# Kernel optimization log

Hardware: AMD Instinct MI355X
Metric: run time of the kernel (lower is better)

## Reference

```python
import jax, jax.numpy as jnp
import numpy as np

NUM_CLASSES = 2
THRESHOLD = 0.35   # overlap_thresh
NEG_POS = 7        # negative:positive mining ratio
VAR0, VAR1 = 0.1, 0.2  # self.variance


def point_form(boxes):
    # (cx,cy,w,h) -> (xmin,ymin,xmax,ymax); boxes [P,4]
    return jnp.concatenate([boxes[:, :2] - boxes[:, 2:] / 2,
                            boxes[:, :2] + boxes[:, 2:] / 2], axis=1)


def jaccard(box_a, box_b):
    # box_a [B,O,4] xyxy, box_b [P,4] xyxy -> IoU [B,O,P]
    max_xy = jnp.minimum(box_a[:, :, None, 2:], box_b[None, None, :, 2:])
    min_xy = jnp.maximum(box_a[:, :, None, :2], box_b[None, None, :, :2])
    wh = jnp.clip(max_xy - min_xy, 0.0)
    inter = wh[..., 0] * wh[..., 1]
    area_a = ((box_a[..., 2] - box_a[..., 0]) * (box_a[..., 3] - box_a[..., 1]))[:, :, None]
    area_b = ((box_b[:, 2] - box_b[:, 0]) * (box_b[:, 3] - box_b[:, 1]))[None, None, :]
    return inter / (area_a + area_b - inter)


def encode(matched, priors):
    # matched [B,P,4] xyxy, priors [1,P,4] cxcywh -> offsets [B,P,4]
    g_cxcy = (matched[..., :2] + matched[..., 2:]) / 2 - priors[..., :2]
    g_cxcy = g_cxcy / (VAR0 * priors[..., 2:])
    g_wh = (matched[..., 2:] - matched[..., :2]) / priors[..., 2:]
    g_wh = jnp.log(g_wh) / VAR1
    return jnp.concatenate([g_cxcy, g_wh], axis=-1)


def match(truths, labels, priors):
    # truths [B,O,4] xyxy, labels [B,O] float, priors [P,4] cxcywh
    overlaps = jaccard(truths, point_form(priors))      # [B,O,P]
    best_prior_idx = jnp.argmax(overlaps, axis=2)       # [B,O] best prior per gt
    best_truth_overlap = jnp.max(overlaps, axis=1)      # [B,P]
    best_truth_idx = jnp.argmax(overlaps, axis=1)       # [B,P] best gt per prior
    O = truths.shape[1]

    def fix(bto, bti, bpi):
        # ensure every gt keeps its best prior (index_fill_ / loop in torch)
        bto = bto.at[bpi].set(2.0)
        bti = bti.at[bpi].set(jnp.arange(O))
        return bto, bti

    best_truth_overlap, best_truth_idx = jax.vmap(fix)(
        best_truth_overlap, best_truth_idx, best_prior_idx)
    matched = jnp.take_along_axis(truths, best_truth_idx[..., None], axis=1)  # [B,P,4]
    conf = jnp.take_along_axis(labels, best_truth_idx, axis=1).astype(jnp.int32) + 1
    conf = jnp.where(best_truth_overlap < THRESHOLD, 0, conf)  # background
    loc = encode(matched, priors[None])
    return loc, conf


def setup_inputs() -> dict:
    key = jax.random.key(0)
    k1, k2, k3, k4, k5, k6 = jax.random.split(key, 6)
    B, P, O, C = 32, 32768, 32, NUM_CLASSES
    loc_data = jax.random.normal(k1, (B, P, 4), jnp.float32)
    conf_data = jax.random.normal(k2, (B, P, C), jnp.float32)
    # priors: (cx,cy,w,h) in [0,1], wh in [0.02,0.3]
    p_cxcy = jax.random.uniform(k3, (P, 2), jnp.float32)
    p_wh = 0.02 + 0.28 * jax.random.uniform(k4, (P, 2), jnp.float32)
    priors = jnp.concatenate([p_cxcy, p_wh], axis=1)
    # targets: valid xyxy boxes + label column (label 0 -> class 1 after +1)
    t_cxcy = 0.1 + 0.8 * jax.random.uniform(k5, (B, O, 2), jnp.float32)
    t_wh = 0.05 + 0.2 * jax.random.uniform(k6, (B, O, 2), jnp.float32)
    boxes = jnp.concatenate([t_cxcy - t_wh / 2, t_cxcy + t_wh / 2], axis=2)
    labels = jnp.zeros((B, O, 1), jnp.float32)
    targets = jnp.concatenate([boxes, labels], axis=2)
    return {"loc_data": loc_data, "conf_data": conf_data,
            "priors": priors, "targets": targets}


def reference(loc_data, conf_data, priors, targets):
    B, P, C = conf_data.shape
    truths = targets[..., :4]
    labels = targets[..., 4]
    loc_t, conf_t = match(truths, labels, priors)   # [B,P,4], [B,P] int
    pos = conf_t > 0                                # [B,P]

    # localization: smooth-L1 summed over positives
    diff = loc_data - loc_t
    ad = jnp.abs(diff)
    sl1 = jnp.where(ad < 1.0, 0.5 * diff * diff, ad - 0.5)
    loss_l = jnp.sum(sl1 * pos[..., None].astype(loc_data.dtype))

    # per-prior CE loss for hard-negative mining
    lse = jax.nn.logsumexp(conf_data, axis=2)                            # [B,P]
    picked = jnp.take_along_axis(conf_data, conf_t[..., None], axis=2)[..., 0]
    ce = lse - picked                                                    # [B,P]
    mine = jnp.where(pos, 0.0, ce)
    # double-argsort rank trick (descending)
    loss_idx = jnp.argsort(-mine, axis=1)
    idx_rank = jnp.argsort(loss_idx, axis=1)
    num_pos = jnp.sum(pos, axis=1, keepdims=True)                        # [B,1]
    num_neg = jnp.minimum(NEG_POS * num_pos, P - 1)
    neg = idx_rank < num_neg

    sel = pos | neg
    loss_c = jnp.sum(jnp.where(sel, ce, 0.0))

    N = jnp.maximum(jnp.sum(num_pos).astype(jnp.float32), 1.0)
    return loss_l / N, loss_c / N
```

## Files before the change

### kernel.cpp

```cpp
#include <hip/hip_runtime.h>
#include <stdint.h>

#define NB 32
#define NP 32768
#define NO 32
#define THRESH 0.35f
#define NT1 64
#define HCOL 33

typedef unsigned long long u64;
typedef unsigned int u32;

__device__ __forceinline__ float iou_corners(float px1, float py1, float px2, float py2, float ab,
                                             float tx1, float ty1, float tx2, float ty2, float aa)
{
#pragma clang fp contract(off)
    float iw = fminf(tx2, px2) - fmaxf(tx1, px1);
    float ih = fminf(ty2, py2) - fmaxf(ty1, py1);
    iw = fmaxf(iw, 0.f); ih = fmaxf(ih, 0.f);
    float inter = iw * ih;
    return __fdividef(inter, aa + ab - inter);
}

__device__ __forceinline__ float smooth_l1_sum(float4 ld, float4 pr, float4 tt)
{
#pragma clang fp contract(off)
    float g0 = __fdividef((tt.x + tt.z) * 0.5f - pr.x, 0.1f * pr.z);
    float g1 = __fdividef((tt.y + tt.w) * 0.5f - pr.y, 0.1f * pr.w);
    float g2 = __logf(__fdividef(tt.z - tt.x, pr.z)) * 5.0f;
    float g3 = __logf(__fdividef(tt.w - tt.y, pr.w)) * 5.0f;
    float d0 = ld.x - g0, d1 = ld.y - g1, d2 = ld.z - g2, d3 = ld.w - g3;
    float a0 = fabsf(d0), a1 = fabsf(d1), a2 = fabsf(d2), a3 = fabsf(d3);
    return (a0 < 1.f ? 0.5f * d0 * d0 : a0 - 0.5f)
         + (a1 < 1.f ? 0.5f * d1 * d1 : a1 - 0.5f)
         + (a2 < 1.f ? 0.5f * d2 * d2 : a2 - 0.5f)
         + (a3 < 1.f ? 0.5f * d3 * d3 : a3 - 0.5f);
}

__device__ __forceinline__ float lse2(float c0, float c1)
{
#pragma clang fp contract(off)
    float mm = fmaxf(c0, c1), mn = fminf(c0, c1);
    return mm + __logf(1.f + __expf(mn - mm));
}

__global__ __launch_bounds__(256) void kern1(
        const float* __restrict__ loc, const float* __restrict__ conf,
        const float* __restrict__ priors, const float* __restrict__ targets,
        float* __restrict__ mine, u64* __restrict__ bpk_part,
        float* __restrict__ part_sl1, float* __restrict__ part_cep, int* __restrict__ part_np,
        float* __restrict__ sl_tot, float* __restrict__ c_tot,
        int* __restrict__ np_tot, int* __restrict__ done_cnt)
{
#pragma clang fp contract(off)
    __shared__ __align__(16) float4 tbc[NO];
    __shared__ float ta[NO], tlab[NO];
    __shared__ u64 keys[NO];
    __shared__ float rs0[4], rs1[4];
    __shared__ int rc[4];
    const int b = blockIdx.y, x = blockIdx.x, tid = threadIdx.x;
    if (b == 0 && x == 0 && tid == 0) {
        *sl_tot = 0.f; *c_tot = 0.f; *np_tot = 0; *done_cnt = 0;
    }
    if (tid < NO * 5) {
        int o = tid / 5, c = tid % 5;
        float v = targets[b * NO * 5 + tid];
        if (c < 4) ((float*)&tbc[o])[c] = v; else tlab[o] = v;
    }
    if (tid < NO) keys[tid] = 0ull;
    __syncthreads();
    if (tid < NO) {
        float4 t = tbc[tid];
        ta[tid] = (t.z - t.x) * (t.w - t.y);
    }
    __syncthreads();

    const int p0 = x * 512 + tid * 2;
    float4 pr[2];
    float px1[2], py1[2], px2[2], py2[2], ab[2];
#pragma unroll
    for (int j = 0; j < 2; ++j) {
        pr[j] = ((const float4*)priors)[p0 + j];
        px1[j] = pr[j].x - pr[j].z * 0.5f;
        py1[j] = pr[j].y - pr[j].w * 0.5f;
        px2[j] = pr[j].x + pr[j].z * 0.5f;
        py2[j] = pr[j].y + pr[j].w * 0.5f;
        ab[j]  = pr[j].z * pr[j].w;
    }
    u64 bk[2] = {0ull, 0ull};
    const int lane_o = tid & 31;
    for (int it = 0; it < NO; ++it) {
        const int o = (it + lane_o) & 31;
        float4 tt = tbc[o];
        float aa = ta[o];
        float iou2[2];
#pragma unroll
        for (int j = 0; j < 2; ++j) {
            float iou = iou_corners(px1[j], py1[j], px2[j], py2[j], ab[j],
                                    tt.x, tt.y, tt.z, tt.w, aa);
            iou2[j] = iou;
            u64 ko = ((u64)__float_as_uint(iou) << 6) | (u64)(63 - o);
            bk[j] = bk[j] > ko ? bk[j] : ko;
        }
        float vm = fmaxf(iou2[0], iou2[1]);
        u64 cur = keys[o];
        if (__float_as_uint(vm) > (u32)(cur >> 32)) {
            float bi = iou2[1]; int bp = p0 + 1;
            if (iou2[0] >= bi) { bi = iou2[0]; bp = p0; }
            atomicMax(&keys[o], ((u64)__float_as_uint(bi) << 32) | (u64)(~(u32)bp));
        }
    }

    const size_t gbase = (size_t)b * NP + p0;
    float4 cf = ((const float4*)conf)[gbase >> 1];
    float c0[2] = {cf.x, cf.z};
    float c1[2] = {cf.y, cf.w};
    float2 mout;
    float s_sl1 = 0.f, s_cep = 0.f;
    int np = 0;
#pragma unroll
    for (int j = 0; j < 2; ++j) {
        u32 vb = (u32)(bk[j] >> 6);
        float bv = __uint_as_float(vb);
        int o = 63 - (int)(bk[j] & 63);
        int cfv = (bv < THRESH) ? 0 : ((int)tlab[o] + 1);
        bool pos = cfv > 0;
        float4 ld = ((const float4*)loc)[gbase + j];
        float sl1 = smooth_l1_sum(ld, pr[j], tbc[o]);
        float ce = lse2(c0[j], c1[j]) - ((cfv == 0) ? c0[j] : c1[j]);
        if (pos) { s_sl1 += sl1; s_cep += ce; np++; }
        ((float*)&mout)[j] = pos ? 0.f : ce;
    }
    ((float2*)mine)[gbase >> 1] = mout;

#pragma unroll
    for (int m = 32; m; m >>= 1) {
        s_sl1 += __shfl_xor(s_sl1, m, 64);
        s_cep += __shfl_xor(s_cep, m, 64);
        np    += __shfl_xor(np, m, 64);
    }
    int lane = tid & 63, w = tid >> 6;
    if (lane == 0) { rs0[w] = s_sl1; rs1[w] = s_cep; rc[w] = np; }
    __syncthreads();
    if (tid == 0) {
        float t0 = 0.f, t1 = 0.f; int t2 = 0;
        for (int i = 0; i < 4; ++i) { t0 += rs0[i]; t1 += rs1[i]; t2 += rc[i]; }
        part_sl1[b * NT1 + x] = t0;
        part_cep[b * NT1 + x] = t1;
        part_np [b * NT1 + x] = t2;
    }
    if (tid < NO) bpk_part[(b * NT1 + x) * 32 + tid] = keys[tid];
}

__global__ __launch_bounds__(1024) void kern3(
        const float* __restrict__ loc, const float* __restrict__ conf,
        const float* __restrict__ priors, const float* __restrict__ targets,
        const u64* __restrict__ bpk_part, const float* __restrict__ mine,
        const float* __restrict__ part_sl1, const float* __restrict__ part_cep,
        const int* __restrict__ part_np,
        float* __restrict__ sl_tot, float* __restrict__ c_tot,
        int* __restrict__ np_tot, int* __restrict__ done_cnt,
        float* __restrict__ out)
{
#pragma clang fp contract(off)
    const int b = blockIdx.x, tid = threadIdx.x;
    const int wave = tid >> 6, lane = tid & 63;
    const int cl = lane & 31;
    __shared__ __align__(16) float4 tbc[NO];
    __shared__ float tlab[NO], tas[NO];
    __shared__ u32 pp[NO];
    __shared__ u32 flags[1024];
    __shared__ int hA[256 * HCOL], hB[256 * HCOL];
    __shared__ int wtot[4];
    __shared__ float rs[16];
    __shared__ int rc2[16];
    __shared__ float sh_sl1, sh_cep;
    __shared__ int sh_np, sh_k, sh_kk;
    __shared__ u32 sh_prefix;

    if (tid < NO * 5) {
        int o = tid / 5, c = tid % 5;
        float v = targets[b * NO * 5 + tid];
        if (c < 4) ((float*)&tbc[o])[c] = v; else tlab[o] = v;
    }
    flags[tid] = 0u;
    for (int i = tid; i < 256 * HCOL; i += 1024) { hA[i] = 0; hB[i] = 0; }

    const float* mb = mine + (size_t)b * NP;
    float v[32];
#pragma unroll
    for (int q = 0; q < 8; ++q) {
        float4 t4 = ((const float4*)mb)[q * 1024 + tid];
        v[4 * q] = t4.x; v[4 * q + 1] = t4.y; v[4 * q + 2] = t4.z; v[4 * q + 3] = t4.w;
    }
    __syncthreads();

#pragma unroll 8
    for (int j = 0; j < 32; ++j)
        atomicAdd(&hA[(__float_as_uint(v[j]) >> 24) * HCOL + cl], 1);
    if (tid < NO) {
        float4 t = tbc[tid];
        tas[tid] = (t.z - t.x) * (t.w - t.y);
        u64 key = 0ull;
        for (int xx = 0; xx < NT1; ++xx) {
            u64 t2 = bpk_part[(b * NT1 + xx) * 32 + tid];
            key = t2 > key ? t2 : key;
        }
        pp[tid] = (key >> 32) ? ~(u32)key : 0u;
    }
    __syncthreads();

    if (tid < NO) {
        const int o = tid;
        const u32 p = pp[o];
        float dsl1 = 0.f, dcep = 0.f; int dnp = 0;
        bool last = true;
        for (int o2 = o + 1; o2 < NO; ++o2)
            if (pp[o2] == p) { last = false; break; }
        if (last) {
            float4 prr = ((const float4*)priors)[p];
            float px1 = prr.x - prr.z * 0.5f, py1 = prr.y - prr.w * 0.5f;
            float px2 = prr.x + prr.z * 0.5f, py2 = prr.y + prr.w * 0.5f;
            float ab = prr.z * prr.w;
            float bv = -1.f; int bo_ = 0;
            for (int o2 = 0; o2 < NO; ++o2) {
                float4 t2 = tbc[o2];
                float i2 = iou_corners(px1, py1, px2, py2, ab, t2.x, t2.y, t2.z, t2.w, tas[o2]);
                if (i2 > bv) { bv = i2; bo_ = o2; }
            }
            int cf_pre = (bv < THRESH) ? 0 : ((int)tlab[bo_] + 1);
            size_t gp = (size_t)b * NP + p;
            float4 ld = ((const float4*)loc)[gp];
            float2 c = ((const float2*)conf)[gp];
            float lse = lse2(c.x, c.y);
            int cf_new = (int)tlab[o] + 1;
            dsl1 = smooth_l1_sum(ld, prr, tbc[o]);
            dcep = lse - ((cf_new == 0) ? c.x : c.y);
            dnp = 1;
            if (cf_pre > 0) {
                dsl1 -= smooth_l1_sum(ld, prr, tbc[bo_]);
                dcep -= lse - ((cf_pre == 0) ? c.x : c.y);
                dnp = 0;
            }
            float oldv = mb[p];
            atomicSub(&hA[(__float_as_uint(oldv) >> 24) * HCOL + cl], 1);
            atomicAdd(&hA[cl], 1);
            atomicOr(&flags[p >> 5], 1u << (p & 31));
        }
        float a = part_sl1[b * NT1 + o] + part_sl1[b * NT1 + 32 + o] + dsl1;
        float d = part_cep[b * NT1 + o] + part_cep[b * NT1 + 32 + o] + dcep;
        int   n = part_np [b * NT1 + o] + part_np [b * NT1 + 32 + o] + dnp;
#pragma unroll
        for (int m = 16; m; m >>= 1) {
            a += __shfl_xor(a, m, 32);
            d += __shfl_xor(d, m, 32);
            n += __shfl_xor(n, m, 32);
        }
        if (o == 0) {
            sh_sl1 = a; sh_cep = d; sh_np = n;
            sh_k = min(7 * n, NP - 1); sh_kk = sh_k; sh_prefix = 0u;
        }
    }
    __syncthreads();

    const int k = sh_k;
    float topk = 0.f;
    if (k > 0) {
#pragma unroll
        for (int q = 0; q < 8; ++q) {
            u32 word = flags[q * 128 + (tid >> 3)];
#pragma unroll
            for (int c = 0; c < 4; ++c)
                if ((word >> (((tid & 7) << 2) + c)) & 1u) v[4 * q + c] = 0.f;
        }
        for (int pass = 0; pass < 4; ++pass) {
            int* cur = (pass & 1) ? hB : hA;
            if (pass > 0) {
                const int shift = 24 - 8 * pass;
                const u32 pfx = sh_prefix;
#pragma unroll 8
                for (int j = 0; j < 32; ++j) {
                    u32 kb = __float_as_uint(v[j]);
                    if ((u32)(((u64)kb) >> (shift + 8)) == pfx)
                        atomicAdd(&cur[((kb >> shift) & 255) * HCOL + cl], 1);
                }
                if (pass < 3) {
                    int* other = (pass & 1) ? hA : hB;
                    for (int i = tid; i < 256 * HCOL; i += 1024) other[i] = 0;
                }
                __syncthreads();
            }
            int tot = 0, suf = 0;
            if (tid < 256) {
                const int hb = tid * HCOL;
#pragma unroll
                for (int i = 0; i < HCOL; ++i) tot += cur[hb + i];
                suf = tot;
#pragma unroll
                for (int off = 1; off < 64; off <<= 1) {
                    int u = __shfl_down(suf, off, 64);
                    if (lane + off < 64) suf += u;
                }
                if (lane == 0) wtot[wave] = suf;
            }
            __syncthreads();
            if (tid < 256) {
                int excl = suf - tot;
                for (int w2 = wave + 1; w2 < 4; ++w2) excl += wtot[w2];
                int kk = sh_kk;
                if (excl < kk && kk <= excl + tot) {
                    sh_prefix = (sh_prefix << 8) | (u32)tid;
                    sh_kk = kk - excl;
                }
            }
            __syncthreads();
        }
        const u32 T = sh_prefix;
        const float tval = __uint_as_float(T);
        float ssum = 0.f; int c2 = 0;
#pragma unroll
        for (int j = 0; j < 32; ++j) {
            if (__float_as_uint(v[j]) > T) { ssum += v[j]; c2++; }
        }
#pragma unroll
        for (int m = 32; m; m >>= 1) {
            ssum += __shfl_xor(ssum, m, 64);
            c2   += __shfl_xor(c2, m, 64);
        }
        if (lane == 0) { rs[wave] = ssum; rc2[wave] = c2; }
        __syncthreads();
        if (tid == 0) {
            float st = 0.f; int ct = 0;
            for (int i = 0; i < 16; ++i) { st += rs[i]; ct += rc2[i]; }
            topk = st + (float)(k - ct) * tval;
        }
    }
    if (tid == 0) {
        atomicAdd(sl_tot, sh_sl1);
        atomicAdd(c_tot, sh_cep + topk);
        atomicAdd(np_tot, sh_np);
        __threadfence();
        int d = atomicAdd(done_cnt, 1);
        if (d == NB - 1) {
            float sl = atomicAdd(sl_tot, 0.f);
            float cc = atomicAdd(c_tot, 0.f);
            int   np = atomicAdd(np_tot, 0);
            float N = fmaxf((float)np, 1.f);
            out[0] = sl / N;
            out[1] = cc / N;
        }
    }
}

extern "C" void kernel_launch(void* const* d_in, const int* in_sizes, int n_in,
                              void* d_out, int out_size, void* d_ws, size_t ws_size,
                              hipStream_t stream) {
    const float* loc     = (const float*)d_in[0];
    const float* conf    = (const float*)d_in[1];
    const float* priors  = (const float*)d_in[2];
    const float* targets = (const float*)d_in[3];
    float* out = (float*)d_out;

    char* ws = (char*)d_ws;
    float* mine     = (float*)ws;
    u64*   bpk_part = (u64*)(ws + 4194304);
    float* part_sl1 = (float*)(ws + 4718592);
    float* part_cep = (float*)(ws + 4726784);
    int*   part_np  = (int*)(ws + 4734976);
    float* sl_tot   = (float*)(ws + 4743168);
    float* c_tot    = (float*)(ws + 4743172);
    int*   np_tot   = (int*)(ws + 4743176);
    int*   done_cnt = (int*)(ws + 4743180);

    dim3 g1(NT1, NB);
    kern1<<<g1, 256, 0, stream>>>(loc, conf, priors, targets, mine, bpk_part,
                                  part_sl1, part_cep, part_np,
                                  sl_tot, c_tot, np_tot, done_cnt);
    kern3<<<NB, 1024, 0, stream>>>(loc, conf, priors, targets, bpk_part, mine,
                                   part_sl1, part_cep, part_np,
                                   sl_tot, c_tot, np_tot, done_cnt, out);
}
```

Before: 127.2 us.

## Overlap per-gt fixup in one wave with histogram clearing in others

Restructures the start of kern3 so that one wave (wave 15) loads targets, reduces the bpk partials with a 64-lane split plus shuffle, and computes the per-gt fixup deltas. Meanwhile the other 15 waves clear the histograms. The forced-match flags are then applied to the mine values before building the first histogram, replacing the old atomic subtract/add correction, and one block-wide barrier is removed. The intent is to take the serial 32-thread section off the critical path. The cost is that all of that work now sits in a single wave.

```diff
diff --git a/kernel.cpp b/kernel.cpp
--- a/kernel.cpp
+++ b/kernel.cpp
@@ -168,9 +168,11 @@
     const int cl = lane & 31;
     __shared__ __align__(16) float4 tbc[NO];
     __shared__ float tlab[NO], tas[NO];
-    __shared__ u32 pp[NO];
+    __shared__ u32 pp_s[NO];
     __shared__ u32 flags[1024];
     __shared__ int hA[256 * HCOL], hB[256 * HCOL];
+    __shared__ float dslA[NO], dceA[NO];
+    __shared__ int dnpA[NO];
     __shared__ int wtot[4];
     __shared__ float rs[16];
     __shared__ int rc2[16];
@@ -178,14 +180,6 @@
     __shared__ int sh_np, sh_k, sh_kk;
     __shared__ u32 sh_prefix;
 
-    if (tid < NO * 5) {
-        int o = tid / 5, c = tid % 5;
-        float v = targets[b * NO * 5 + tid];
-        if (c < 4) ((float*)&tbc[o])[c] = v; else tlab[o] = v;
-    }
-    flags[tid] = 0u;
-    for (int i = tid; i < 256 * HCOL; i += 1024) { hA[i] = 0; hB[i] = 0; }
-
     const float* mb = mine + (size_t)b * NP;
     float v[32];
 #pragma unroll
@@ -193,70 +187,103 @@
         float4 t4 = ((const float4*)mb)[q * 1024 + tid];
         v[4 * q] = t4.x; v[4 * q + 1] = t4.y; v[4 * q + 2] = t4.z; v[4 * q + 3] = t4.w;
     }
+
+    if (wave < 15) {
+        for (int i = tid; i < 1024; i += 960) { }
+        for (int i = tid; i < 256 * HCOL; i += 960) { hA[i] = 0; hB[i] = 0; }
+    } else {
+        for (int i = lane; i < 1024; i += 64) flags[i] = 0u;
+        float tv0 = targets[b * NO * 5 + lane];
+        float tv1 = targets[b * NO * 5 + 64 + lane];
+        float tv2 = (lane < 32) ? targets[b * NO * 5 + 128 + lane] : 0.f;
+        const int ro = lane & 31, rh = lane >> 5;
+        const u64* bp = bpk_part + ((size_t)(b * NT1 + rh * 32)) * 32 + ro;
+        u64 key = 0ull;
+#pragma unroll
+        for (int j = 0; j < 32; ++j) {
+            u64 t2 = bp[(size_t)j * 32];
+            key = t2 > key ? t2 : key;
+        }
+        {
+            int e = lane;       int o = e / 5, c = e % 5;
+            if (c < 4) ((float*)&tbc[o])[c] = tv0; else tlab[o] = tv0;
+            e = lane + 64;      o = e / 5;  c = e % 5;
+            if (c < 4) ((float*)&tbc[o])[c] = tv1; else tlab[o] = tv1;
+            if (lane < 32) {
+                e = lane + 128; o = e / 5;  c = e % 5;
+                if (c < 4) ((float*)&tbc[o])[c] = tv2; else tlab[o] = tv2;
+            }
+        }
+        if (lane < NO) {
+            float4 t = tbc[lane];
+            tas[lane] = (t.z - t.x) * (t.w - t.y);
+        }
+        {
+            u64 t2 = __shfl_xor(key, 32, 64);
+            key = t2 > key ? t2 : key;
+        }
+        u32 ppv = (key >> 32) ? ~(u32)key : 0u;
+        if (lane < NO) pp_s[lane] = ppv;
+        if (lane < NO) {
+            const int o = lane;
+            const u32 p = ppv;
+            float dsl1 = 0.f, dcep = 0.f; int dnp = 0;
+            bool last = true;
+            for (int o2 = o + 1; o2 < NO; ++o2)
+                if (pp_s[o2] == p) { last = false; break; }
+            if (last) {
+                float4 prr = ((const float4*)priors)[p];
+                float px1 = prr.x - prr.z * 0.5f, py1 = prr.y - prr.w * 0.5f;
+                float px2 = prr.x + prr.z * 0.5f, py2 = prr.y + prr.w * 0.5f;
+                float ab = prr.z * prr.w;
+                float bv = -1.f; int bo_ = 0;
+                for (int o2 = 0; o2 < NO; ++o2) {
+                    float4 t2 = tbc[o2];
+                    float i2 = iou_corners(px1, py1, px2, py2, ab, t2.x, t2.y, t2.z, t2.w, tas[o2]);
+                    if (i2 > bv) { bv = i2; bo_ = o2; }
+                }
+                int cf_pre = (bv < THRESH) ? 0 : ((int)tlab[bo_] + 1);
+                size_t gp = (size_t)b * NP + p;
+                float4 ld = ((const float4*)loc)[gp];
+                float2 c = ((const float2*)conf)[gp];
+                float lse = lse2(c.x, c.y);
+                int cf_new = (int)tlab[o] + 1;
+                dsl1 = smooth_l1_sum(ld, prr, tbc[o]);
+                dcep = lse - ((cf_new == 0) ? c.x : c.y);
+                dnp = 1;
+                if (cf_pre > 0) {
+                    dsl1 -= smooth_l1_sum(ld, prr, tbc[bo_]);
+                    dcep -= lse - ((cf_pre == 0) ? c.x : c.y);
+                    dnp = 0;
+                }
+                atomicOr(&flags[p >> 5], 1u << (p & 31));
+            }
+            dslA[o] = dsl1; dceA[o] = dcep; dnpA[o] = dnp;
+        }
+    }
     __syncthreads();
 
+#pragma unroll
+    for (int q = 0; q < 8; ++q) {
+        u32 word = flags[q * 128 + (tid >> 3)];
+#pragma unroll
+        for (int c = 0; c < 4; ++c)
+            if ((word >> (((tid & 7) << 2) + c)) & 1u) v[4 * q + c] = 0.f;
+    }
 #pragma unroll 8
     for (int j = 0; j < 32; ++j)
         atomicAdd(&hA[(__float_as_uint(v[j]) >> 24) * HCOL + cl], 1);
     if (tid < NO) {
-        float4 t = tbc[tid];
-        tas[tid] = (t.z - t.x) * (t.w - t.y);
-        u64 key = 0ull;
-        for (int xx = 0; xx < NT1; ++xx) {
-            u64 t2 = bpk_part[(b * NT1 + xx) * 32 + tid];
-            key = t2 > key ? t2 : key;
-        }
-        pp[tid] = (key >> 32) ? ~(u32)key : 0u;
-    }
-    __syncthreads();
-
-    if (tid < NO) {
-        const int o = tid;
-        const u32 p = pp[o];
-        float dsl1 = 0.f, dcep = 0.f; int dnp = 0;
-        bool last = true;
-        for (int o2 = o + 1; o2 < NO; ++o2)
-            if (pp[o2] == p) { last = false; break; }
-        if (last) {
-            float4 prr = ((const float4*)priors)[p];
-            float px1 = prr.x - prr.z * 0.5f, py1 = prr.y - prr.w * 0.5f;
-            float px2 = prr.x + prr.z * 0.5f, py2 = prr.y + prr.w * 0.5f;
-            float ab = prr.z * prr.w;
-            float bv = -1.f; int bo_ = 0;
-            for (int o2 = 0; o2 < NO; ++o2) {
-                float4 t2 = tbc[o2];
-                float i2 = iou_corners(px1, py1, px2, py2, ab, t2.x, t2.y, t2.z, t2.w, tas[o2]);
-                if (i2 > bv) { bv = i2; bo_ = o2; }
-            }
-            int cf_pre = (bv < THRESH) ? 0 : ((int)tlab[bo_] + 1);
-            size_t gp = (size_t)b * NP + p;
-            float4 ld = ((const float4*)loc)[gp];
-            float2 c = ((const float2*)conf)[gp];
-            float lse = lse2(c.x, c.y);
-            int cf_new = (int)tlab[o] + 1;
-            dsl1 = smooth_l1_sum(ld, prr, tbc[o]);
-            dcep = lse - ((cf_new == 0) ? c.x : c.y);
-            dnp = 1;
-            if (cf_pre > 0) {
-                dsl1 -= smooth_l1_sum(ld, prr, tbc[bo_]);
-                dcep -= lse - ((cf_pre == 0) ? c.x : c.y);
-                dnp = 0;
-            }
-            float oldv = mb[p];
-            atomicSub(&hA[(__float_as_uint(oldv) >> 24) * HCOL + cl], 1);
-            atomicAdd(&hA[cl], 1);
-            atomicOr(&flags[p >> 5], 1u << (p & 31));
-        }
-        float a = part_sl1[b * NT1 + o] + part_sl1[b * NT1 + 32 + o] + dsl1;
-        float d = part_cep[b * NT1 + o] + part_cep[b * NT1 + 32 + o] + dcep;
-        int   n = part_np [b * NT1 + o] + part_np [b * NT1 + 32 + o] + dnp;
+        float a = part_sl1[b * NT1 + tid] + part_sl1[b * NT1 + 32 + tid] + dslA[tid];
+        float d = part_cep[b * NT1 + tid] + part_cep[b * NT1 + 32 + tid] + dceA[tid];
+        int   n = part_np [b * NT1 + tid] + part_np [b * NT1 + 32 + tid] + dnpA[tid];
 #pragma unroll
         for (int m = 16; m; m >>= 1) {
             a += __shfl_xor(a, m, 32);
             d += __shfl_xor(d, m, 32);
             n += __shfl_xor(n, m, 32);
         }
-        if (o == 0) {
+        if (tid == 0) {
             sh_sl1 = a; sh_cep = d; sh_np = n;
             sh_k = min(7 * n, NP - 1); sh_kk = sh_k; sh_prefix = 0u;
         }
@@ -266,13 +293,6 @@
     const int k = sh_k;
     float topk = 0.f;
     if (k > 0) {
-#pragma unroll
-        for (int q = 0; q < 8; ++q) {
-            u32 word = flags[q * 128 + (tid >> 3)];
-#pragma unroll
-            for (int c = 0; c < 4; ++c)
-                if ((word >> (((tid & 7) << 2) + c)) & 1u) v[4 * q + c] = 0.f;
-        }
         for (int pass = 0; pass < 4; ++pass) {
             int* cur = (pass & 1) ? hB : hA;
             if (pass > 0) {
```

Result: no change. 126.3 us (-0.7%).

## Fuse match and hard-negative top-k kernels via last-block-per-batch completion counter

Applied to the files above, without the earlier changes.

Merges the per-prior matching kernel and the per-batch top-k selection kernel into one launch. Each 1024-thread block covers four 512-prior tiles, and the last block to finish a batch (found with an atomic counter) runs the radix-select top-k by re-reading the mining buffer from global memory instead of holding it in registers. Loc loads are also skipped for non-positive priors, and counters are cleared with a memset. The aim is to remove the second launch and the inter-kernel gap, at the cost of large shared memory per block (lower occupancy in the matching phase), repeated global reads during radix passes, and a serialized tail per batch.

```diff
diff --git a/kernel.cpp b/kernel.cpp
--- a/kernel.cpp
+++ b/kernel.cpp
@@ -6,10 +6,14 @@
 #define NO 32
 #define THRESH 0.35f
 #define NT1 64
+#define GR 16
 #define HCOL 33
 
 typedef unsigned long long u64;
 typedef unsigned int u32;
+
+#define AGLD(p)    __hip_atomic_load((p), __ATOMIC_RELAXED, __HIP_MEMORY_SCOPE_AGENT)
+#define AGST(p, v) __hip_atomic_store((p), (v), __ATOMIC_RELAXED, __HIP_MEMORY_SCOPE_AGENT)
 
 __device__ __forceinline__ float iou_corners(float px1, float py1, float px2, float py2, float ab,
                                              float tx1, float ty1, float tx2, float ty2, float aa)
@@ -44,38 +48,46 @@
     return mm + __logf(1.f + __expf(mn - mm));
 }
 
-__global__ __launch_bounds__(256) void kern1(
+__global__ __launch_bounds__(1024) void kfused(
         const float* __restrict__ loc, const float* __restrict__ conf,
         const float* __restrict__ priors, const float* __restrict__ targets,
         float* __restrict__ mine, u64* __restrict__ bpk_part,
         float* __restrict__ part_sl1, float* __restrict__ part_cep, int* __restrict__ part_np,
         float* __restrict__ sl_tot, float* __restrict__ c_tot,
-        int* __restrict__ np_tot, int* __restrict__ done_cnt)
+        int* __restrict__ np_tot, int* __restrict__ done_cnt,
+        int* __restrict__ batch_cnt, float* __restrict__ out)
 {
 #pragma clang fp contract(off)
     __shared__ __align__(16) float4 tbc[NO];
-    __shared__ float ta[NO], tlab[NO];
-    __shared__ u64 keys[NO];
-    __shared__ float rs0[4], rs1[4];
-    __shared__ int rc[4];
-    const int b = blockIdx.y, x = blockIdx.x, tid = threadIdx.x;
-    if (b == 0 && x == 0 && tid == 0) {
-        *sl_tot = 0.f; *c_tot = 0.f; *np_tot = 0; *done_cnt = 0;
-    }
+    __shared__ float tlab[NO], tas[NO];
+    __shared__ u64 keys[4][NO];
+    __shared__ float rs0[16], rs1[16];
+    __shared__ int rc[16];
+    __shared__ __align__(16) int hA[256 * HCOL];
+    __shared__ __align__(16) int hB[256 * HCOL];
+    __shared__ u32 flags[1024];
+    __shared__ u32 pp_s[NO];
+    __shared__ int wtot[4];
+    __shared__ float rs[16];
+    __shared__ int rc2[16];
+    __shared__ float sh_sl1, sh_cep;
+    __shared__ int sh_np, sh_k, sh_kk, sh_done;
+    __shared__ u32 sh_prefix;
+
+    const int b = blockIdx.y, g = blockIdx.x, tid = threadIdx.x;
+    const int unit = tid >> 8, ut = tid & 255;
+    const int x = g * 4 + unit;
+    const int lane = tid & 63, wv = tid >> 6;
+
     if (tid < NO * 5) {
         int o = tid / 5, c = tid % 5;
         float v = targets[b * NO * 5 + tid];
         if (c < 4) ((float*)&tbc[o])[c] = v; else tlab[o] = v;
     }
-    if (tid < NO) keys[tid] = 0ull;
-    __syncthreads();
-    if (tid < NO) {
-        float4 t = tbc[tid];
-        ta[tid] = (t.z - t.x) * (t.w - t.y);
-    }
-    __syncthreads();
-
-    const int p0 = x * 512 + tid * 2;
+    if (tid < NO * 4) ((u64*)keys)[tid] = 0ull;
+    __syncthreads();
+
+    const int p0 = x * 512 + ut * 2;
     float4 pr[2];
     float px1[2], py1[2], px2[2], py2[2], ab[2];
 #pragma unroll
@@ -88,11 +100,11 @@
         ab[j]  = pr[j].z * pr[j].w;
     }
     u64 bk[2] = {0ull, 0ull};
-    const int lane_o = tid & 31;
+    const int lane_o = ut & 31;
     for (int it = 0; it < NO; ++it) {
         const int o = (it + lane_o) & 31;
         float4 tt = tbc[o];
-        float aa = ta[o];
+        float aa = (tt.z - tt.x) * (tt.w - tt.y);
         float iou2[2];
 #pragma unroll
         for (int j = 0; j < 2; ++j) {
@@ -103,11 +115,11 @@
             bk[j] = bk[j] > ko ? bk[j] : ko;
         }
         float vm = fmaxf(iou2[0], iou2[1]);
-        u64 cur = keys[o];
+        u64 cur = keys[unit][o];
         if (__float_as_uint(vm) > (u32)(cur >> 32)) {
             float bi = iou2[1]; int bp = p0 + 1;
             if (iou2[0] >= bi) { bi = iou2[0]; bp = p0; }
-            atomicMax(&keys[o], ((u64)__float_as_uint(bi) << 32) | (u64)(~(u32)bp));
+            atomicMax(&keys[unit][o], ((u64)__float_as_uint(bi) << 32) | (u64)(~(u32)bp));
         }
     }
 
@@ -115,7 +127,7 @@
     float4 cf = ((const float4*)conf)[gbase >> 1];
     float c0[2] = {cf.x, cf.z};
     float c1[2] = {cf.y, cf.w};
-    float2 mout;
+    float mo0 = 0.f, mo1 = 0.f;
     float s_sl1 = 0.f, s_cep = 0.f;
     int np = 0;
 #pragma unroll
@@ -125,13 +137,17 @@
         int o = 63 - (int)(bk[j] & 63);
         int cfv = (bv < THRESH) ? 0 : ((int)tlab[o] + 1);
         bool pos = cfv > 0;
-        float4 ld = ((const float4*)loc)[gbase + j];
-        float sl1 = smooth_l1_sum(ld, pr[j], tbc[o]);
         float ce = lse2(c0[j], c1[j]) - ((cfv == 0) ? c0[j] : c1[j]);
-        if (pos) { s_sl1 += sl1; s_cep += ce; np++; }
-        ((float*)&mout)[j] = pos ? 0.f : ce;
-    }
-    ((float2*)mine)[gbase >> 1] = mout;
+        if (pos) {
+            float4 ld = ((const float4*)loc)[gbase + j];
+            s_sl1 += smooth_l1_sum(ld, pr[j], tbc[o]);
+            s_cep += ce;
+            np++;
+        }
+        if (j == 0) mo0 = pos ? 0.f : ce; else mo1 = pos ? 0.f : ce;
+    }
+    AGST((u64*)mine + (gbase >> 1),
+         ((u64)__float_as_uint(mo0)) | (((u64)__float_as_uint(mo1)) << 32));
 
 #pragma unroll
     for (int m = 32; m; m >>= 1) {
@@ -139,93 +155,58 @@
         s_cep += __shfl_xor(s_cep, m, 64);
         np    += __shfl_xor(np, m, 64);
     }
-    int lane = tid & 63, w = tid >> 6;
-    if (lane == 0) { rs0[w] = s_sl1; rs1[w] = s_cep; rc[w] = np; }
+    if (lane == 0) { rs0[wv] = s_sl1; rs1[wv] = s_cep; rc[wv] = np; }
+    __syncthreads();
+    if (ut == 0) {
+        float t0 = 0.f, t1 = 0.f; int t2 = 0;
+        for (int i = 0; i < 4; ++i) { t0 += rs0[unit * 4 + i]; t1 += rs1[unit * 4 + i]; t2 += rc[unit * 4 + i]; }
+        AGST(&part_sl1[b * NT1 + x], t0);
+        AGST(&part_cep[b * NT1 + x], t1);
+        AGST(&part_np [b * NT1 + x], t2);
+    }
+    if (ut < NO) AGST(&bpk_part[(b * NT1 + x) * 32 + ut], keys[unit][ut]);
     __syncthreads();
     if (tid == 0) {
-        float t0 = 0.f, t1 = 0.f; int t2 = 0;
-        for (int i = 0; i < 4; ++i) { t0 += rs0[i]; t1 += rs1[i]; t2 += rc[i]; }
-        part_sl1[b * NT1 + x] = t0;
-        part_cep[b * NT1 + x] = t1;
-        part_np [b * NT1 + x] = t2;
-    }
-    if (tid < NO) bpk_part[(b * NT1 + x) * 32 + tid] = keys[tid];
-}
-
-__global__ __launch_bounds__(1024) void kern3(
-        const float* __restrict__ loc, const float* __restrict__ conf,
-        const float* __restrict__ priors, const float* __restrict__ targets,
-        const u64* __restrict__ bpk_part, const float* __restrict__ mine,
-        const float* __restrict__ part_sl1, const float* __restrict__ part_cep,
-        const int* __restrict__ part_np,
-        float* __restrict__ sl_tot, float* __restrict__ c_tot,
-        int* __restrict__ np_tot, int* __restrict__ done_cnt,
-        float* __restrict__ out)
-{
-#pragma clang fp contract(off)
-    const int b = blockIdx.x, tid = threadIdx.x;
-    const int wave = tid >> 6, lane = tid & 63;
-    const int cl = lane & 31;
-    __shared__ __align__(16) float4 tbc[NO];
-    __shared__ float tlab[NO], tas[NO];
-    __shared__ u32 pp[NO];
-    __shared__ u32 flags[1024];
-    __shared__ int hA[256 * HCOL], hB[256 * HCOL];
-    __shared__ int wtot[4];
-    __shared__ float rs[16];
-    __shared__ int rc2[16];
-    __shared__ float sh_sl1, sh_cep;
-    __shared__ int sh_np, sh_k, sh_kk;
-    __shared__ u32 sh_prefix;
-
-    if (tid < NO * 5) {
-        int o = tid / 5, c = tid % 5;
-        float v = targets[b * NO * 5 + tid];
-        if (c < 4) ((float*)&tbc[o])[c] = v; else tlab[o] = v;
-    }
+        __threadfence();
+        sh_done = atomicAdd(&batch_cnt[b], 1);
+    }
+    __syncthreads();
+    if (sh_done != GR - 1) return;
+    __threadfence();
+
     flags[tid] = 0u;
-    for (int i = tid; i < 256 * HCOL; i += 1024) { hA[i] = 0; hB[i] = 0; }
-
-    const float* mb = mine + (size_t)b * NP;
-    float v[32];
-#pragma unroll
-    for (int q = 0; q < 8; ++q) {
-        float4 t4 = ((const float4*)mb)[q * 1024 + tid];
-        v[4 * q] = t4.x; v[4 * q + 1] = t4.y; v[4 * q + 2] = t4.z; v[4 * q + 3] = t4.w;
-    }
-    __syncthreads();
-
-#pragma unroll 8
-    for (int j = 0; j < 32; ++j)
-        atomicAdd(&hA[(__float_as_uint(v[j]) >> 24) * HCOL + cl], 1);
+    for (int i = tid; i < 256 * HCOL; i += 1024) hA[i] = 0;
+    {
+        u64* scr = (u64*)hB;
+        int o = tid & 31, ch = tid >> 5;
+        u64 a = AGLD(&bpk_part[(b * NT1 + 2 * ch) * 32 + o]);
+        u64 c2 = AGLD(&bpk_part[(b * NT1 + 2 * ch + 1) * 32 + o]);
+        scr[o * 32 + ch] = a > c2 ? a : c2;
+    }
+    __syncthreads();
     if (tid < NO) {
+        u64* scr = (u64*)hB;
+        u64 key = 0ull;
+        for (int ch = 0; ch < 32; ++ch) { u64 t2 = scr[tid * 32 + ch]; key = t2 > key ? t2 : key; }
         float4 t = tbc[tid];
         tas[tid] = (t.z - t.x) * (t.w - t.y);
-        u64 key = 0ull;
-        for (int xx = 0; xx < NT1; ++xx) {
-            u64 t2 = bpk_part[(b * NT1 + xx) * 32 + tid];
-            key = t2 > key ? t2 : key;
-        }
-        pp[tid] = (key >> 32) ? ~(u32)key : 0u;
-    }
-    __syncthreads();
-
-    if (tid < NO) {
+        u32 ppv = (key >> 32) ? ~(u32)key : 0u;
+        pp_s[tid] = ppv;
         const int o = tid;
-        const u32 p = pp[o];
+        const u32 p = ppv;
         float dsl1 = 0.f, dcep = 0.f; int dnp = 0;
         bool last = true;
         for (int o2 = o + 1; o2 < NO; ++o2)
-            if (pp[o2] == p) { last = false; break; }
+            if (pp_s[o2] == p) { last = false; break; }
         if (last) {
             float4 prr = ((const float4*)priors)[p];
-            float px1 = prr.x - prr.z * 0.5f, py1 = prr.y - prr.w * 0.5f;
-            float px2 = prr.x + prr.z * 0.5f, py2 = prr.y + prr.w * 0.5f;
-            float ab = prr.z * prr.w;
+            float qx1 = prr.x - prr.z * 0.5f, qy1 = prr.y - prr.w * 0.5f;
+            float qx2 = prr.x + prr.z * 0.5f, qy2 = prr.y + prr.w * 0.5f;
+            float qab = prr.z * prr.w;
             float bv = -1.f; int bo_ = 0;
             for (int o2 = 0; o2 < NO; ++o2) {
                 float4 t2 = tbc[o2];
-                float i2 = iou_corners(px1, py1, px2, py2, ab, t2.x, t2.y, t2.z, t2.w, tas[o2]);
+                float i2 = iou_corners(qx1, qy1, qx2, qy2, qab, t2.x, t2.y, t2.z, t2.w, tas[o2]);
                 if (i2 > bv) { bv = i2; bo_ = o2; }
             }
             int cf_pre = (bv < THRESH) ? 0 : ((int)tlab[bo_] + 1);
@@ -242,14 +223,11 @@
                 dcep -= lse - ((cf_pre == 0) ? c.x : c.y);
                 dnp = 0;
             }
-            float oldv = mb[p];
-            atomicSub(&hA[(__float_as_uint(oldv) >> 24) * HCOL + cl], 1);
-            atomicAdd(&hA[cl], 1);
             atomicOr(&flags[p >> 5], 1u << (p & 31));
         }
-        float a = part_sl1[b * NT1 + o] + part_sl1[b * NT1 + 32 + o] + dsl1;
-        float d = part_cep[b * NT1 + o] + part_cep[b * NT1 + 32 + o] + dcep;
-        int   n = part_np [b * NT1 + o] + part_np [b * NT1 + 32 + o] + dnp;
+        float a = AGLD(&part_sl1[b * NT1 + o]) + AGLD(&part_sl1[b * NT1 + 32 + o]) + dsl1;
+        float d = AGLD(&part_cep[b * NT1 + o]) + AGLD(&part_cep[b * NT1 + 32 + o]) + dcep;
+        int   n = AGLD(&part_np [b * NT1 + o]) + AGLD(&part_np [b * NT1 + 32 + o]) + dnp;
 #pragma unroll
         for (int m = 16; m; m >>= 1) {
             a += __shfl_xor(a, m, 32);
@@ -264,29 +242,46 @@
     __syncthreads();
 
     const int k = sh_k;
+    const u64* m64 = (const u64*)mine + (size_t)b * (NP / 2);
+    const int cl = lane & 31;
     float topk = 0.f;
     if (k > 0) {
-#pragma unroll
+        for (int i = tid; i < 256 * HCOL; i += 1024) hB[i] = 0;
         for (int q = 0; q < 8; ++q) {
+            u64 w0 = AGLD(&m64[q * 2048 + 2 * tid]);
+            u64 w1 = AGLD(&m64[q * 2048 + 2 * tid + 1]);
             u32 word = flags[q * 128 + (tid >> 3)];
-#pragma unroll
-            for (int c = 0; c < 4; ++c)
-                if ((word >> (((tid & 7) << 2) + c)) & 1u) v[4 * q + c] = 0.f;
-        }
+            float f[4] = { __uint_as_float((u32)w0), __uint_as_float((u32)(w0 >> 32)),
+                           __uint_as_float((u32)w1), __uint_as_float((u32)(w1 >> 32)) };
+#pragma unroll
+            for (int c = 0; c < 4; ++c) {
+                if ((word >> (((tid & 7) << 2) + c)) & 1u) f[c] = 0.f;
+                atomicAdd(&hA[(__float_as_uint(f[c]) >> 24) * HCOL + cl], 1);
+            }
+        }
+        __syncthreads();
         for (int pass = 0; pass < 4; ++pass) {
             int* cur = (pass & 1) ? hB : hA;
             if (pass > 0) {
                 const int shift = 24 - 8 * pass;
                 const u32 pfx = sh_prefix;
-#pragma unroll 8
-                for (int j = 0; j < 32; ++j) {
-                    u32 kb = __float_as_uint(v[j]);
-                    if ((u32)(((u64)kb) >> (shift + 8)) == pfx)
-                        atomicAdd(&cur[((kb >> shift) & 255) * HCOL + cl], 1);
+                for (int q = 0; q < 8; ++q) {
+                    u64 w0 = AGLD(&m64[q * 2048 + 2 * tid]);
+                    u64 w1 = AGLD(&m64[q * 2048 + 2 * tid + 1]);
+                    u32 word = flags[q * 128 + (tid >> 3)];
+                    float f[4] = { __uint_as_float((u32)w0), __uint_as_float((u32)(w0 >> 32)),
+                                   __uint_as_float((u32)w1), __uint_as_float((u32)(w1 >> 32)) };
+#pragma unroll
+                    for (int c = 0; c < 4; ++c) {
+                        if ((word >> (((tid & 7) << 2) + c)) & 1u) f[c] = 0.f;
+                        u32 kb = __float_as_uint(f[c]);
+                        if ((u32)(((u64)kb) >> (shift + 8)) == pfx)
+                            atomicAdd(&cur[((kb >> shift) & 255) * HCOL + cl], 1);
+                    }
                 }
                 if (pass < 3) {
-                    int* other = (pass & 1) ? hA : hB;
-                    for (int i = tid; i < 256 * HCOL; i += 1024) other[i] = 0;
+                    int* oth = (pass & 1) ? hA : hB;
+                    for (int i = tid; i < 256 * HCOL; i += 1024) oth[i] = 0;
                 }
                 __syncthreads();
             }
@@ -301,12 +296,12 @@
                     int u = __shfl_down(suf, off, 64);
                     if (lane + off < 64) suf += u;
                 }
-                if (lane == 0) wtot[wave] = suf;
+                if (lane == 0) wtot[wv] = suf;
             }
             __syncthreads();
             if (tid < 256) {
                 int excl = suf - tot;
-                for (int w2 = wave + 1; w2 < 4; ++w2) excl += wtot[w2];
+                for (int w2 = wv + 1; w2 < 4; ++w2) excl += wtot[w2];
                 int kk = sh_kk;
                 if (excl < kk && kk <= excl + tot) {
                     sh_prefix = (sh_prefix << 8) | (u32)tid;
@@ -318,16 +313,24 @@
         const u32 T = sh_prefix;
         const float tval = __uint_as_float(T);
         float ssum = 0.f; int c2 = 0;
-#pragma unroll
-        for (int j = 0; j < 32; ++j) {
-            if (__float_as_uint(v[j]) > T) { ssum += v[j]; c2++; }
+        for (int q = 0; q < 8; ++q) {
+            u64 w0 = AGLD(&m64[q * 2048 + 2 * tid]);
+            u64 w1 = AGLD(&m64[q * 2048 + 2 * tid + 1]);
+            u32 word = flags[q * 128 + (tid >> 3)];
+            float f[4] = { __uint_as_float((u32)w0), __uint_as_float((u32)(w0 >> 32)),
+                           __uint_as_float((u32)w1), __uint_as_float((u32)(w1 >> 32)) };
+#pragma unroll
+            for (int c = 0; c < 4; ++c) {
+                if ((word >> (((tid & 7) << 2) + c)) & 1u) f[c] = 0.f;
+                if (__float_as_uint(f[c]) > T) { ssum += f[c]; c2++; }
+            }
         }
 #pragma unroll
         for (int m = 32; m; m >>= 1) {
             ssum += __shfl_xor(ssum, m, 64);
             c2   += __shfl_xor(c2, m, 64);
         }
-        if (lane == 0) { rs[wave] = ssum; rc2[wave] = c2; }
+        if (lane == 0) { rs[wv] = ssum; rc2[wv] = c2; }
         __syncthreads();
         if (tid == 0) {
             float st = 0.f; int ct = 0;
@@ -344,8 +347,8 @@
         if (d == NB - 1) {
             float sl = atomicAdd(sl_tot, 0.f);
             float cc = atomicAdd(c_tot, 0.f);
-            int   np = atomicAdd(np_tot, 0);
-            float N = fmaxf((float)np, 1.f);
+            int   nptot = atomicAdd(np_tot, 0);
+            float N = fmaxf((float)nptot, 1.f);
             out[0] = sl / N;
             out[1] = cc / N;
         }
@@ -371,12 +374,12 @@
     float* c_tot    = (float*)(ws + 4743172);
     int*   np_tot   = (int*)(ws + 4743176);
     int*   done_cnt = (int*)(ws + 4743180);
-
-    dim3 g1(NT1, NB);
-    kern1<<<g1, 256, 0, stream>>>(loc, conf, priors, targets, mine, bpk_part,
-                                  part_sl1, part_cep, part_np,
-                                  sl_tot, c_tot, np_tot, done_cnt);
-    kern3<<<NB, 1024, 0, stream>>>(loc, conf, priors, targets, bpk_part, mine,
-                                   part_sl1, part_cep, part_np,
-                                   sl_tot, c_tot, np_tot, done_cnt, out);
-}
+    int*   batch_cnt= (int*)(ws + 4743184);
+
+    hipMemsetAsync(ws + 4743168, 0, 144, stream);
+
+    dim3 grd(GR, NB);
+    kfused<<<grd, 1024, 0, stream>>>(loc, conf, priors, targets, mine, bpk_part,
+                                     part_sl1, part_cep, part_np,
+                                     sl_tot, c_tot, np_tot, done_cnt, batch_cnt, out);
+}
```

After: 178.4 us. 40.2% more time.
